# Kernel optimization log

Hardware: AMD Instinct MI355X
Metric: run time of the kernel (lower is better)

## Reference

```python
import jax, jax.numpy as jnp
import numpy as np

HID = 512
ALPHA = 0.01
PI = np.float32(np.pi)


def _mlp(x, W0, b0, W1, b1, W2, b2, W3, b3):
    # x: [..., 2] -> scalar field u(x): [...]
    h = jnp.tanh(x @ W0 + b0)
    h = jnp.tanh(h @ W1 + b1)
    h = jnp.tanh(h @ W2 + b2)
    return (h @ W3 + b3)[..., 0]


def _forcing(x):
    # f = -Delta u for u = sin(pi x) sin(pi y^2)
    xx, yy = x[:, 0], x[:, 1]
    return (-PI ** 2 * (1 + 4 * yy ** 2) * jnp.sin(PI * xx) * jnp.sin(PI * yy ** 2)
            + 2 * PI * jnp.sin(PI * xx) * jnp.cos(PI * yy ** 2))


def setup_inputs() -> dict:
    key = jax.random.key(0)
    ks = jax.random.split(key, 6)
    n_i, n_b = 20000, 800
    x_interior = jax.random.uniform(ks[0], (n_i, 2), dtype=jnp.float32)  # domain (0,1)
    theta = jnp.linspace(0.0, 2.0 * np.pi, n_b)
    x_boundary = jnp.stack([(jnp.cos(theta) + 1.0) * 0.5,
                            (jnp.sin(theta) + 1.0) * 0.5], axis=1).astype(jnp.float32)

    def w(k, shape, fan_in):
        return (jax.random.normal(k, shape, jnp.float32) / np.float32(np.sqrt(fan_in)))

    W0 = w(ks[1], (2, HID), 2)
    b0 = jnp.zeros((HID,), jnp.float32)
    W1 = w(ks[2], (HID, HID), HID)
    b1 = jnp.zeros((HID,), jnp.float32)
    W2 = w(ks[3], (HID, HID), HID)
    b2 = jnp.zeros((HID,), jnp.float32)
    W3 = w(ks[4], (HID, 1), HID)
    b3 = jnp.zeros((1,), jnp.float32)
    return dict(x_interior=x_interior, x_boundary=x_boundary,
                W0=W0, b0=b0, W1=W1, b1=b1, W2=W2, b2=b2, W3=W3, b3=b3)


def reference(x_interior, x_boundary, W0, b0, W1, b1, W2, b2, W3, b3):
    params = (W0, b0, W1, b1, W2, b2, W3, b3)

    def u_scalar(x):  # x: [2] -> scalar
        return _mlp(x, *params)

    g = jax.grad(u_scalar)

    def lap_one(x):
        # Laplacian = trace of Hessian via forward-over-reverse HVPs
        lap = jnp.float32(0.0)
        for i in range(2):
            e = jnp.zeros((2,), x.dtype).at[i].set(1.0)
            _, hv = jax.jvp(g, (x,), (e,))
            lap = lap + hv[i]
        return lap

    laplacian = jax.vmap(lap_one)(x_interior)  # [n_interior]
    interior_loss = jnp.mean((laplacian - _forcing(x_interior)) ** 2)
    boundary_loss = jnp.mean(_mlp(x_boundary, *params) ** 2)
    total_loss = ALPHA * interior_loss + boundary_loss
    return total_loss, interior_loss, boundary_loss
```

## Files before the change

### kernel.cpp

```cpp
#include <hip/hip_runtime.h>
#include <math.h>

#define HID 512
#define PPB 32
#define SLAB 512

typedef __attribute__((ext_vector_type(8))) _Float16 half8;
typedef __attribute__((ext_vector_type(4))) _Float16 half4;
typedef __attribute__((ext_vector_type(4))) float f32x4;

static __device__ __forceinline__ float fast_tanh(float x) {
    float e = __expf(2.f * x);
    return 1.f - 2.f / (e + 1.f);
}


__global__ __launch_bounds__(256) void prep_wt(
    const float* __restrict__ W1, const float* __restrict__ W2,
    _Float16* __restrict__ W1h, _Float16* __restrict__ W2h)
{
    __shared__ float T[64][65];
    int b = blockIdx.x;
    const float* W = (b < 64) ? W1 : W2;
    _Float16* Wh   = (b < 64) ? W1h : W2h;
    int tb = b & 63;
    int jbG = tb >> 3, kbG = tb & 7;
    int j0 = jbG * 64, k0 = kbG * 64;
    int t = threadIdx.x;
    #pragma unroll
    for (int r = 0; r < 16; ++r) {
        int kl = r * 4 + (t >> 6);
        int jl = t & 63;
        T[kl][jl] = W[(size_t)(k0 + kl) * HID + j0 + jl];
    }
    __syncthreads();
    int ljb = t >> 6;
    int l15 = (t >> 2) & 15;
    int quad = t & 3;
    #pragma unroll
    for (int lkb = 0; lkb < 2; ++lkb) {
        half8 v;
        #pragma unroll
        for (int k8 = 0; k8 < 8; ++k8)
            v[k8] = (_Float16)T[lkb * 32 + quad * 8 + k8][ljb * 16 + l15];
        size_t out = (size_t)((jbG * 4 + ljb) * 16 + (kbG * 2 + lkb)) * SLAB
                   + (quad * 16 + l15) * 8;
        *(half8*)(Wh + out) = v;
    }
}

template<bool FULL>
static __device__ __forceinline__ void layer_pass(
    const _Float16* __restrict__ Wh, const float* __restrict__ bias,
    _Float16* Als, int wv, int lane)
{
    const int l15 = lane & 15, quad = lane >> 4;
    const int pf  = wv >> 3;
    const int jg  = wv & 7;
    const int j0w = jg * 64;
    const int jb0 = jg * 4;
    const int loff = lane * 8;

    f32x4 acc[4][4];
    #pragma unroll
    for (int s = 0; s < 4; ++s)
        #pragma unroll
        for (int jt = 0; jt < 4; ++jt) acc[s][jt] = (f32x4)0.f;

    half8 w[2][4];
    #pragma unroll
    for (int jt = 0; jt < 4; ++jt)
        w[0][jt] = *(const half8*)(Wh + (size_t)((jb0 + jt) * 16 + 0) * SLAB + loff);

    #pragma unroll 2
    for (int kb = 0; kb < 16; ++kb) {
        const int cb = kb & 1, nb = cb ^ 1;
        half8 a[4];
        #pragma unroll
        for (int s = 0; s < 4; ++s)
            a[s] = *(const half8*)(Als + ((s * 2 + pf) * 16 + kb) * SLAB + loff);
        if (kb + 1 < 16) {
            #pragma unroll
            for (int jt = 0; jt < 4; ++jt)
                w[nb][jt] = *(const half8*)(Wh + (size_t)((jb0 + jt) * 16 + kb + 1) * SLAB + loff);
        }
        #pragma unroll
        for (int s = 0; s < 4; ++s)
            #pragma unroll
            for (int jt = 0; jt < 4; ++jt)
                acc[s][jt] = __builtin_amdgcn_mfma_f32_16x16x32_f16(
                    w[cb][jt], a[s], acc[s][jt], 0, 0, 0);
    }

    __syncthreads();

    #pragma unroll
    for (int jt = 0; jt < 4; ++jt) {
        const int jbase = j0w + jt * 16 + quad * 4;
        const int okb = jbase >> 5;
        const int qo  = (jbase & 31) >> 3;
        const int e0  = (quad & 1) * 4;
        f32x4 bv = *(const f32x4*)&bias[jbase];
        half4 vh, vt1, vt2, vS;
        #pragma unroll
        for (int r = 0; r < 4; ++r) {
            float a  = fast_tanh(acc[0][jt][r] + bv[r]);
            float g  = 1.f - a * a;
            float z1 = acc[1][jt][r];
            float z2 = acc[2][jt][r];
            vh[r] = (_Float16)a;
            if (FULL) {
                vt1[r] = (_Float16)(g * z1);
                vt2[r] = (_Float16)(g * z2);
            }
            vS[r] = (_Float16)(g * acc[3][jt][r] - 2.f * a * g * (z1 * z1 + z2 * z2));
        }
        const int ooff = (qo * 16 + l15) * 8 + e0;
        *(half4*)(Als + ((0 * 2 + pf) * 16 + okb) * SLAB + ooff) = vh;
        if (FULL) {
            *(half4*)(Als + ((1 * 2 + pf) * 16 + okb) * SLAB + ooff) = vt1;
            *(half4*)(Als + ((2 * 2 + pf) * 16 + okb) * SLAB + ooff) = vt2;
        }
        *(half4*)(Als + ((3 * 2 + pf) * 16 + okb) * SLAB + ooff) = vS;
    }
    __syncthreads();
}

__global__ __launch_bounds__(1024, 4) void pois_fused(
    const float* __restrict__ x_int, const float* __restrict__ x_bnd,
    const float* __restrict__ W0, const float* __restrict__ b0,
    const _Float16* __restrict__ W1h, const float* __restrict__ b1,
    const _Float16* __restrict__ W2h, const float* __restrict__ b2,
    const float* __restrict__ W3, const float* __restrict__ b3,
    float* __restrict__ partials, int NI, int NT, int nblk)
{
    __shared__ _Float16 Als[8 * 16 * SLAB];
    __shared__ float scU[16][32], scL[16][32], sc[64];

    const int tid = threadIdx.x;
    const int wv = tid >> 6, lane = tid & 63;
    const int l15 = lane & 15, quad = lane >> 4;
    const int p0 = blockIdx.x * PPB;

    #pragma unroll
    for (int ph = 0; ph < 2; ++ph) {
        const int p = ph * 16 + l15;
        int gp = p0 + p;
        int gpc = (gp >= NT) ? 0 : gp;
        float xx, yy;
        if (gpc < NI) { xx = x_int[2 * gpc];        yy = x_int[2 * gpc + 1]; }
        else          { xx = x_bnd[2 * (gpc - NI)]; yy = x_bnd[2 * (gpc - NI) + 1]; }
        const int k = wv * 32 + quad * 8;
        f32x4 w0a = *(const f32x4*)&W0[k],       w0b = *(const f32x4*)&W0[k + 4];
        f32x4 w1a = *(const f32x4*)&W0[HID + k], w1b = *(const f32x4*)&W0[HID + k + 4];
        f32x4 b0a = *(const f32x4*)&b0[k],       b0b = *(const f32x4*)&b0[k + 4];
        half8 vh, vt1, vt2, vS;
        #pragma unroll
        for (int e = 0; e < 8; ++e) {
            float w0i = (e < 4) ? w0a[e] : w0b[e - 4];
            float w1i = (e < 4) ? w1a[e] : w1b[e - 4];
            float bbi = (e < 4) ? b0a[e] : b0b[e - 4];
            float a = fast_tanh(xx * w0i + yy * w1i + bbi);
            float g = 1.f - a * a;
            vh[e]  = (_Float16)a;
            vt1[e] = (_Float16)(g * w0i);
            vt2[e] = (_Float16)(g * w1i);
            vS[e]  = (_Float16)(-2.f * a * g * (w0i * w0i + w1i * w1i));
        }
        const int off = lane * 8;
        *(half8*)(Als + ((0 * 2 + ph) * 16 + wv) * SLAB + off) = vh;
        *(half8*)(Als + ((1 * 2 + ph) * 16 + wv) * SLAB + off) = vt1;
        *(half8*)(Als + ((2 * 2 + ph) * 16 + wv) * SLAB + off) = vt2;
        *(half8*)(Als + ((3 * 2 + ph) * 16 + wv) * SLAB + off) = vS;
    }
    __syncthreads();

    layer_pass<true >(W1h, b1, Als, wv, lane);
    layer_pass<false>(W2h, b2, Als, wv, lane);

    {
        const int k = wv * 32 + quad * 8;
        f32x4 wa = *(const f32x4*)&W3[k], wb = *(const f32x4*)&W3[k + 4];
        #pragma unroll
        for (int ph = 0; ph < 2; ++ph) {
            half8 hh = *(const half8*)(Als + ((0 * 2 + ph) * 16 + wv) * SLAB + lane * 8);
            half8 ss = *(const half8*)(Als + ((3 * 2 + ph) * 16 + wv) * SLAB + lane * 8);
            float u = 0.f, lap = 0.f;
            #pragma unroll
            for (int e = 0; e < 4; ++e) {
                u   += (float)hh[e] * wa[e] + (float)hh[e + 4] * wb[e];
                lap += (float)ss[e] * wa[e] + (float)ss[e + 4] * wb[e];
            }
            u   += __shfl_xor(u, 16);   u   += __shfl_xor(u, 32);
            lap += __shfl_xor(lap, 16); lap += __shfl_xor(lap, 32);
            if (lane < 16) { scU[wv][ph * 16 + lane] = u; scL[wv][ph * 16 + lane] = lap; }
        }
    }
    __syncthreads();
    if (tid < 32) {
        const int p = tid;
        float u = 0.f, lap = 0.f;
        #pragma unroll
        for (int w = 0; w < 16; ++w) { u += scU[w][p]; lap += scL[w][p]; }
        int gp = p0 + p;
        float vi = 0.f, vb = 0.f;
        if (gp < NI) {
            const float PIf = 3.14159265358979323846f;
            float xx = x_int[2 * gp], yy = x_int[2 * gp + 1];
            float sx = sinf(PIf * xx);
            float y2 = yy * yy;
            float sy = sinf(PIf * y2), cy = cosf(PIf * y2);
            float f = -PIf * PIf * (1.f + 4.f * y2) * sx * sy + 2.f * PIf * sx * cy;
            float r = lap - f;
            vi = r * r;
        } else if (gp < NT) {
            float uu = u + b3[0];
            vb = uu * uu;
        }
        sc[p * 2] = vi; sc[p * 2 + 1] = vb;
    }
    __syncthreads();
    if (tid == 0) {
        float svi = 0.f, svb = 0.f;
        #pragma unroll
        for (int p = 0; p < PPB; ++p) { svi += sc[p * 2]; svb += sc[p * 2 + 1]; }
        partials[blockIdx.x] = svi;
        partials[nblk + blockIdx.x] = svb;
    }
}

__global__ __launch_bounds__(256) void pois_reduce(
    const float* __restrict__ partials, float* __restrict__ out,
    int nblk, int NI, int NB)
{
    int tid = threadIdx.x;
    float si = 0.f, sb = 0.f;
    for (int i = tid; i < nblk; i += 256) {
        si += partials[i];
        sb += partials[nblk + i];
    }
    #pragma unroll
    for (int off = 32; off > 0; off >>= 1) {
        si += __shfl_xor(si, off);
        sb += __shfl_xor(sb, off);
    }
    __shared__ float ri[4], rb[4];
    int wv = tid >> 6;
    if ((tid & 63) == 0) { ri[wv] = si; rb[wv] = sb; }
    __syncthreads();
    if (tid == 0) {
        float inter = (ri[0] + ri[1] + ri[2] + ri[3]) / (float)NI;
        float bound = (rb[0] + rb[1] + rb[2] + rb[3]) / (float)NB;
        out[0] = 0.01f * inter + bound;
        out[1] = inter;
        out[2] = bound;
    }
}

extern "C" void kernel_launch(void* const* d_in, const int* in_sizes, int n_in,
                              void* d_out, int out_size, void* d_ws, size_t ws_size,
                              hipStream_t stream)
{
    const float* x_int = (const float*)d_in[0];
    const float* x_bnd = (const float*)d_in[1];
    const float* W0 = (const float*)d_in[2];
    const float* b0 = (const float*)d_in[3];
    const float* W1 = (const float*)d_in[4];
    const float* b1 = (const float*)d_in[5];
    const float* W2 = (const float*)d_in[6];
    const float* b2 = (const float*)d_in[7];
    const float* W3 = (const float*)d_in[8];
    const float* b3 = (const float*)d_in[9];

    int NI = in_sizes[0] / 2;
    int NB = in_sizes[1] / 2;
    int NT = NI + NB;
    int nblk = (NT + PPB - 1) / PPB;

    float* partials = (float*)d_ws;
    _Float16* W1h = (_Float16*)((char*)d_ws + 16384);
    _Float16* W2h = W1h + 262144;

    prep_wt<<<128, 256, 0, stream>>>(W1, W2, W1h, W2h);

    pois_fused<<<nblk, 1024, 0, stream>>>(
        x_int, x_bnd, W0, b0, W1h, b1, W2h, b2, W3, b3,
        partials, NI, NT, nblk);

    pois_reduce<<<1, 256, 0, stream>>>(partials, (float*)d_out, nblk, NI, NB);
}
```

Before: 185.2 us.

## Halve points per block to 16 with 512-thread blocks

```diff
diff --git a/kernel.cpp b/kernel.cpp
--- a/kernel.cpp
+++ b/kernel.cpp
@@ -2,7 +2,7 @@
 #include <math.h>
 
 #define HID 512
-#define PPB 32
+#define PPB 16
 #define SLAB 512
 
 typedef __attribute__((ext_vector_type(8))) _Float16 half8;
@@ -55,10 +55,8 @@
     _Float16* Als, int wv, int lane)
 {
     const int l15 = lane & 15, quad = lane >> 4;
-    const int pf  = wv >> 3;
-    const int jg  = wv & 7;
-    const int j0w = jg * 64;
-    const int jb0 = jg * 4;
+    const int j0w = wv * 64;
+    const int jb0 = wv * 4;
     const int loff = lane * 8;
 
     f32x4 acc[4][4];
@@ -78,7 +76,7 @@
         half8 a[4];
         #pragma unroll
         for (int s = 0; s < 4; ++s)
-            a[s] = *(const half8*)(Als + ((s * 2 + pf) * 16 + kb) * SLAB + loff);
+            a[s] = *(const half8*)(Als + (s * 16 + kb) * SLAB + loff);
         if (kb + 1 < 16) {
             #pragma unroll
             for (int jt = 0; jt < 4; ++jt)
@@ -116,17 +114,17 @@
             vS[r] = (_Float16)(g * acc[3][jt][r] - 2.f * a * g * (z1 * z1 + z2 * z2));
         }
         const int ooff = (qo * 16 + l15) * 8 + e0;
-        *(half4*)(Als + ((0 * 2 + pf) * 16 + okb) * SLAB + ooff) = vh;
+        *(half4*)(Als + (0 * 16 + okb) * SLAB + ooff) = vh;
         if (FULL) {
-            *(half4*)(Als + ((1 * 2 + pf) * 16 + okb) * SLAB + ooff) = vt1;
-            *(half4*)(Als + ((2 * 2 + pf) * 16 + okb) * SLAB + ooff) = vt2;
-        }
-        *(half4*)(Als + ((3 * 2 + pf) * 16 + okb) * SLAB + ooff) = vS;
-    }
-    __syncthreads();
-}
-
-__global__ __launch_bounds__(1024, 4) void pois_fused(
+            *(half4*)(Als + (1 * 16 + okb) * SLAB + ooff) = vt1;
+            *(half4*)(Als + (2 * 16 + okb) * SLAB + ooff) = vt2;
+        }
+        *(half4*)(Als + (3 * 16 + okb) * SLAB + ooff) = vS;
+    }
+    __syncthreads();
+}
+
+__global__ __launch_bounds__(512, 4) void pois_fused(
     const float* __restrict__ x_int, const float* __restrict__ x_bnd,
     const float* __restrict__ W0, const float* __restrict__ b0,
     const _Float16* __restrict__ W1h, const float* __restrict__ b1,
@@ -134,44 +132,47 @@
     const float* __restrict__ W3, const float* __restrict__ b3,
     float* __restrict__ partials, int NI, int NT, int nblk)
 {
-    __shared__ _Float16 Als[8 * 16 * SLAB];
-    __shared__ float scU[16][32], scL[16][32], sc[64];
+    __shared__ _Float16 Als[4 * 16 * SLAB];
+    __shared__ float scU[8][16], scL[8][16], sc[32];
 
     const int tid = threadIdx.x;
     const int wv = tid >> 6, lane = tid & 63;
     const int l15 = lane & 15, quad = lane >> 4;
     const int p0 = blockIdx.x * PPB;
 
-    #pragma unroll
-    for (int ph = 0; ph < 2; ++ph) {
-        const int p = ph * 16 + l15;
+    {
+        const int p = l15;
         int gp = p0 + p;
         int gpc = (gp >= NT) ? 0 : gp;
         float xx, yy;
         if (gpc < NI) { xx = x_int[2 * gpc];        yy = x_int[2 * gpc + 1]; }
         else          { xx = x_bnd[2 * (gpc - NI)]; yy = x_bnd[2 * (gpc - NI) + 1]; }
-        const int k = wv * 32 + quad * 8;
-        f32x4 w0a = *(const f32x4*)&W0[k],       w0b = *(const f32x4*)&W0[k + 4];
-        f32x4 w1a = *(const f32x4*)&W0[HID + k], w1b = *(const f32x4*)&W0[HID + k + 4];
-        f32x4 b0a = *(const f32x4*)&b0[k],       b0b = *(const f32x4*)&b0[k + 4];
-        half8 vh, vt1, vt2, vS;
-        #pragma unroll
-        for (int e = 0; e < 8; ++e) {
-            float w0i = (e < 4) ? w0a[e] : w0b[e - 4];
-            float w1i = (e < 4) ? w1a[e] : w1b[e - 4];
-            float bbi = (e < 4) ? b0a[e] : b0b[e - 4];
-            float a = fast_tanh(xx * w0i + yy * w1i + bbi);
-            float g = 1.f - a * a;
-            vh[e]  = (_Float16)a;
-            vt1[e] = (_Float16)(g * w0i);
-            vt2[e] = (_Float16)(g * w1i);
-            vS[e]  = (_Float16)(-2.f * a * g * (w0i * w0i + w1i * w1i));
-        }
-        const int off = lane * 8;
-        *(half8*)(Als + ((0 * 2 + ph) * 16 + wv) * SLAB + off) = vh;
-        *(half8*)(Als + ((1 * 2 + ph) * 16 + wv) * SLAB + off) = vt1;
-        *(half8*)(Als + ((2 * 2 + ph) * 16 + wv) * SLAB + off) = vt2;
-        *(half8*)(Als + ((3 * 2 + ph) * 16 + wv) * SLAB + off) = vS;
+        #pragma unroll
+        for (int i = 0; i < 2; ++i) {
+            const int kb = wv * 2 + i;
+            const int k = kb * 32 + quad * 8;
+            f32x4 w0a = *(const f32x4*)&W0[k],       w0b = *(const f32x4*)&W0[k + 4];
+            f32x4 w1a = *(const f32x4*)&W0[HID + k], w1b = *(const f32x4*)&W0[HID + k + 4];
+            f32x4 b0a = *(const f32x4*)&b0[k],       b0b = *(const f32x4*)&b0[k + 4];
+            half8 vh, vt1, vt2, vS;
+            #pragma unroll
+            for (int e = 0; e < 8; ++e) {
+                float w0i = (e < 4) ? w0a[e] : w0b[e - 4];
+                float w1i = (e < 4) ? w1a[e] : w1b[e - 4];
+                float bbi = (e < 4) ? b0a[e] : b0b[e - 4];
+                float a = fast_tanh(xx * w0i + yy * w1i + bbi);
+                float g = 1.f - a * a;
+                vh[e]  = (_Float16)a;
+                vt1[e] = (_Float16)(g * w0i);
+                vt2[e] = (_Float16)(g * w1i);
+                vS[e]  = (_Float16)(-2.f * a * g * (w0i * w0i + w1i * w1i));
+            }
+            const int off = lane * 8;
+            *(half8*)(Als + (0 * 16 + kb) * SLAB + off) = vh;
+            *(half8*)(Als + (1 * 16 + kb) * SLAB + off) = vt1;
+            *(half8*)(Als + (2 * 16 + kb) * SLAB + off) = vt2;
+            *(half8*)(Als + (3 * 16 + kb) * SLAB + off) = vS;
+        }
     }
     __syncthreads();
 
@@ -179,29 +180,30 @@
     layer_pass<false>(W2h, b2, Als, wv, lane);
 
     {
-        const int k = wv * 32 + quad * 8;
-        f32x4 wa = *(const f32x4*)&W3[k], wb = *(const f32x4*)&W3[k + 4];
-        #pragma unroll
-        for (int ph = 0; ph < 2; ++ph) {
-            half8 hh = *(const half8*)(Als + ((0 * 2 + ph) * 16 + wv) * SLAB + lane * 8);
-            half8 ss = *(const half8*)(Als + ((3 * 2 + ph) * 16 + wv) * SLAB + lane * 8);
-            float u = 0.f, lap = 0.f;
+        float u = 0.f, lap = 0.f;
+        #pragma unroll
+        for (int i = 0; i < 2; ++i) {
+            const int kb = wv * 2 + i;
+            const int k = kb * 32 + quad * 8;
+            half8 hh = *(const half8*)(Als + (0 * 16 + kb) * SLAB + lane * 8);
+            half8 ss = *(const half8*)(Als + (3 * 16 + kb) * SLAB + lane * 8);
+            f32x4 wa = *(const f32x4*)&W3[k], wb = *(const f32x4*)&W3[k + 4];
             #pragma unroll
             for (int e = 0; e < 4; ++e) {
                 u   += (float)hh[e] * wa[e] + (float)hh[e + 4] * wb[e];
                 lap += (float)ss[e] * wa[e] + (float)ss[e + 4] * wb[e];
             }
-            u   += __shfl_xor(u, 16);   u   += __shfl_xor(u, 32);
-            lap += __shfl_xor(lap, 16); lap += __shfl_xor(lap, 32);
-            if (lane < 16) { scU[wv][ph * 16 + lane] = u; scL[wv][ph * 16 + lane] = lap; }
-        }
-    }
-    __syncthreads();
-    if (tid < 32) {
+        }
+        u   += __shfl_xor(u, 16);   u   += __shfl_xor(u, 32);
+        lap += __shfl_xor(lap, 16); lap += __shfl_xor(lap, 32);
+        if (lane < 16) { scU[wv][lane] = u; scL[wv][lane] = lap; }
+    }
+    __syncthreads();
+    if (tid < 16) {
         const int p = tid;
         float u = 0.f, lap = 0.f;
         #pragma unroll
-        for (int w = 0; w < 16; ++w) { u += scU[w][p]; lap += scL[w][p]; }
+        for (int w = 0; w < 8; ++w) { u += scU[w][p]; lap += scL[w][p]; }
         int gp = p0 + p;
         float vi = 0.f, vb = 0.f;
         if (gp < NI) {
@@ -283,7 +285,7 @@
 
     prep_wt<<<128, 256, 0, stream>>>(W1, W2, W1h, W2h);
 
-    pois_fused<<<nblk, 1024, 0, stream>>>(
+    pois_fused<<<nblk, 512, 0, stream>>>(
         x_int, x_bnd, W0, b0, W1h, b1, W2h, b2, W3, b3,
         partials, NI, NT, nblk);
 
```

Result: no change. 182.4 us (-1.5%).
